# Kernel tuning notes

Hardware: AMD Instinct MI355X
Metric: run time of the kernel (lower is better)

## Reference

```python
import jax, jax.numpy as jnp
import numpy as np

B, S, D = 4, 4096, 1024
E, C, F = 8, 1024, 2048


def setup_inputs() -> dict:
    key = jax.random.key(0)
    ks = jax.random.split(key, 6)
    # weight init per module: uniform(-bound, bound), bound = sqrt(3)*sqrt(1/3)/sqrt(fan_in) = 1/sqrt(fan_in)
    b_d = 1.0 / np.sqrt(D)
    b_f = 1.0 / np.sqrt(F)
    return {
        "x": jax.random.normal(ks[0], (B, S, D), dtype=jnp.float32),
        "expert_weights": jax.random.uniform(ks[1], (B, E, C), dtype=jnp.float32),
        "token_indices": jax.random.randint(ks[2], (B, E, C), 0, S, dtype=jnp.int64),
        "w1": jax.random.uniform(ks[3], (E, D, F), dtype=jnp.float32, minval=-b_d, maxval=b_d),
        "w2": jax.random.uniform(ks[4], (E, D, F), dtype=jnp.float32, minval=-b_d, maxval=b_d),
        "w3": jax.random.uniform(ks[5], (E, F, D), dtype=jnp.float32, minval=-b_f, maxval=b_f),
    }


def reference(x, expert_weights, token_indices, w1, w2, w3):
    # gather: each expert picks `capacity` tokens from its batch row
    b_idx = jnp.arange(B)[:, None, None]                      # (B,1,1)
    expert_inputs = x[b_idx, token_indices]                   # (B,E,C,D)
    # grouped swiglu FFN per expert (no weight repeat needed: einsum batches over E)
    gate = jax.nn.silu(jnp.einsum('becd,edf->becf', expert_inputs, w1))
    value = jnp.einsum('becd,edf->becf', expert_inputs, w2)
    expert_outputs = jnp.einsum('becf,efd->becd', gate * value, w3)  # (B,E,C,D)
    weighted = expert_outputs * expert_weights[..., None]     # (B,E,C,D)
    # weighted scatter-add combine back to (B,S,D)
    out = jnp.zeros((B, S, D), dtype=x.dtype)
    out = out.at[b_idx, token_indices].add(weighted)
    return out
```

## Files before the change

### kernel.cpp

```cpp
#include <hip/hip_runtime.h>

#define Bn 4
#define Sn 4096
#define Dn 1024
#define En 8
#define Cn 1024
#define Fn 2048
#define Mn (Bn * Cn)

typedef __bf16 bf16x4 __attribute__((ext_vector_type(4)));
typedef __bf16 bf16x8 __attribute__((ext_vector_type(8)));
typedef float f32x4 __attribute__((ext_vector_type(4)));

#define GLOAD16(gsrc, ldst)                                                    \
  __builtin_amdgcn_global_load_lds(                                            \
      (const __attribute__((address_space(1))) void*)(gsrc),                   \
      (__attribute__((address_space(3))) void*)(ldst), 16, 0, 0)

#define VMCNT(n) asm volatile("s_waitcnt vmcnt(" #n ")" ::: "memory")
#define SCHEDB() __builtin_amdgcn_sched_barrier(0)

__global__ __launch_bounds__(256) void tcast_kernel(
    const float* __restrict__ in, __bf16* __restrict__ out, int K, int N) {
  __shared__ float t[32][33];
  const int e = blockIdx.z;
  const float* src = in + (size_t)e * K * N;
  __bf16* dst = out + (size_t)e * K * N;
  const int n0 = blockIdx.x << 5, k0 = blockIdx.y << 5;
  const int tx = threadIdx.x & 31, ty = threadIdx.x >> 5;
#pragma unroll
  for (int i = 0; i < 4; ++i)
    t[ty + i * 8][tx] = src[(size_t)(k0 + ty + i * 8) * N + (n0 + tx)];
  __syncthreads();
#pragma unroll
  for (int i = 0; i < 4; ++i)
    dst[(size_t)(n0 + ty + i * 8) * K + (k0 + tx)] = (__bf16)t[tx][ty + i * 8];
}

__global__ __launch_bounds__(256) void gather_cast_kernel(
    const float* __restrict__ x, const int* __restrict__ tok,
    __bf16* __restrict__ Xg) {
  const int gid = blockIdx.x * 4 + (threadIdx.x >> 6);
  const int lane = threadIdx.x & 63;
  const int e = gid >> 12, m = gid & 4095, b = m >> 10, c = m & 1023;
  const int t = tok[((size_t)b * En + e) * Cn + c];
  const float* src = x + ((size_t)b * Sn + t) * Dn;
  __bf16* dst = Xg + (size_t)gid * Dn;
#pragma unroll
  for (int i = 0; i < 4; ++i) {
    f32x4 v = *(const f32x4*)(src + i * 256 + lane * 4);
    bf16x4 o;
    o[0] = (__bf16)v[0];
    o[1] = (__bf16)v[1];
    o[2] = (__bf16)v[2];
    o[3] = (__bf16)v[3];
    *(bf16x4*)(dst + i * 256 + lane * 4) = o;
  }
}

__global__ __launch_bounds__(512, 2) void gemm12_kernel(
    const __bf16* __restrict__ Xg, const float* __restrict__ ew,
    const __bf16* __restrict__ w1T, const __bf16* __restrict__ w2T,
    __bf16* __restrict__ Hbh, int e0) {
  __shared__ __align__(16) char lds[131072];
  __bf16* As = (__bf16*)lds;
  __bf16* Bs = (__bf16*)(lds + 65536);
  float* xch = (float*)lds;

  const int tid = threadIdx.x;
  const int lane = tid & 63, wid = tid >> 6;
  const int wr = wid >> 2, wc = wid & 3;
  const int mt = blockIdx.x, ft = blockIdx.y, eLoc = blockIdx.z;
  const int e = e0 + eLoc;

  const int srow = tid >> 2;
  const int sof = ((tid & 3) ^ ((tid >> 3) & 3)) << 3;

  const __bf16* pA0 = Xg + ((size_t)e * Mn + mt * 256 + srow) * Dn + sof;
  const __bf16* pA1 = pA0 + (size_t)128 * Dn;
  const __bf16* pB0 = w1T + ((size_t)e * Fn + ft * 128 + srow) * Dn + sof;
  const __bf16* pB1 = w2T + ((size_t)e * Fn + ft * 128 + srow) * Dn + sof;

  f32x4 acc[8][4];
  const f32x4 z4 = {0.f, 0.f, 0.f, 0.f};
#pragma unroll
  for (int i = 0; i < 8; ++i)
#pragma unroll
    for (int j = 0; j < 4; ++j) acc[i][j] = z4;

  auto stage = [&](int kt) {
    const int buf = kt & 3;
    const int ko = kt << 5;
    GLOAD16(pA0 + ko, As + buf * 8192 + wid * 512);
    GLOAD16(pA1 + ko, As + buf * 8192 + 4096 + wid * 512);
    GLOAD16(pB0 + ko, Bs + buf * 8192 + wid * 512);
    GLOAD16(pB1 + ko, Bs + buf * 8192 + 4096 + wid * 512);
  };

  const int kb = lane >> 4, rl = lane & 15;
  auto compute = [&](int buf) {
    const __bf16* Ab = As + buf * 8192;
    const __bf16* Bb = Bs + buf * 8192;
    bf16x8 a8[8], b8[4];
#pragma unroll
    for (int fm = 0; fm < 8; ++fm) {
      const int r = wr * 128 + fm * 16 + rl;
      a8[fm] = *(const bf16x8*)(Ab + r * 32 + ((kb ^ ((r >> 1) & 3)) << 3));
    }
#pragma unroll
    for (int fn = 0; fn < 4; ++fn) {
      const int r = wc * 64 + fn * 16 + rl;
      b8[fn] = *(const bf16x8*)(Bb + r * 32 + ((kb ^ ((r >> 1) & 3)) << 3));
    }
    __builtin_amdgcn_s_setprio(1);
#pragma unroll
    for (int fm = 0; fm < 8; ++fm)
#pragma unroll
      for (int fn = 0; fn < 4; ++fn)
        acc[fm][fn] = __builtin_amdgcn_mfma_f32_16x16x32_bf16(
            a8[fm], b8[fn], acc[fm][fn], 0, 0, 0);
    __builtin_amdgcn_s_setprio(0);
  };

  const int KT = Dn / 32;
  stage(0);
  stage(1);
  stage(2);
#pragma unroll 1
  for (int kt = 0; kt < KT; ++kt) {
    SCHEDB();
    if (kt < KT - 2)
      VMCNT(8);
    else if (kt == KT - 2)
      VMCNT(4);
    else
      VMCNT(0);
    __builtin_amdgcn_s_barrier();
    SCHEDB();
    if (kt + 3 < KT) stage(kt + 3);
    compute(kt & 3);
  }

  __syncthreads();
  const int rl0 = (lane >> 4) << 2, cl = lane & 15;
  if (wc >= 2) {
    float* reg = xch + (wr * 2 + (wc - 2)) * 8192;
#pragma unroll
    for (int fm = 0; fm < 8; ++fm)
#pragma unroll
      for (int fn = 0; fn < 4; ++fn)
#pragma unroll
        for (int j = 0; j < 4; ++j) {
          const int row = fm * 16 + rl0 + j;
          reg[row * 64 + ((fn ^ ((row >> 2) & 3)) << 4) + cl] = acc[fm][fn][j];
        }
  }
  __syncthreads();
  if (wc < 2) {
    const float* reg = xch + (wr * 2 + wc) * 8192;
    const int m0 = mt * 256 + wr * 128;
    const int b = m0 >> 10;
    const size_t ewBase = ((size_t)b * En + e) * Cn;
    __bf16* hOut =
        Hbh + ((size_t)eLoc * Mn + m0) * Fn + ft * 128 + wc * 64;
#pragma unroll
    for (int fm = 0; fm < 8; ++fm)
#pragma unroll
      for (int j = 0; j < 4; ++j) {
        const int rloc = fm * 16 + rl0 + j;
        const float wgt = ew[ewBase + ((m0 + rloc) & (Cn - 1))];
#pragma unroll
        for (int fn = 0; fn < 4; ++fn) {
          const float g = acc[fm][fn][j];
          const float v = reg[rloc * 64 + ((fn ^ ((rloc >> 2) & 3)) << 4) + cl];
          const float h = (g / (1.f + __expf(-g))) * v * wgt;
          hOut[(size_t)rloc * Fn + fn * 16 + cl] = (__bf16)h;
        }
      }
  }
}

__global__ __launch_bounds__(512, 2) void gemm3_kernel(
    const __bf16* __restrict__ Hbh, const __bf16* __restrict__ w3T,
    const int* __restrict__ tok, float* __restrict__ out, int e0) {
  __shared__ __align__(16) char lds[131072];
  __bf16* As = (__bf16*)lds;
  __bf16* Bs = (__bf16*)(lds + 65536);

  const int tid = threadIdx.x;
  const int lane = tid & 63, wid = tid >> 6;
  const int wr = wid >> 2, wc = wid & 3;
  const int mt = blockIdx.x, nt = blockIdx.y, eLoc = blockIdx.z;
  const int e = e0 + eLoc;

  const int srow = tid >> 2;
  const int sof = ((tid & 3) ^ ((tid >> 3) & 3)) << 3;

  const __bf16* pA0 = Hbh + ((size_t)eLoc * Mn + mt * 256 + srow) * Fn + sof;
  const __bf16* pA1 = pA0 + (size_t)128 * Fn;
  const __bf16* pB0 = w3T + ((size_t)e * Dn + nt * 256 + srow) * Fn + sof;
  const __bf16* pB1 = pB0 + (size_t)128 * Fn;

  f32x4 acc[8][4];
  const f32x4 z4 = {0.f, 0.f, 0.f, 0.f};
#pragma unroll
  for (int i = 0; i < 8; ++i)
#pragma unroll
    for (int j = 0; j < 4; ++j) acc[i][j] = z4;

  auto stage = [&](int kt) {
    const int buf = kt & 3;
    const int ko = kt << 5;
    GLOAD16(pA0 + ko, As + buf * 8192 + wid * 512);
    GLOAD16(pA1 + ko, As + buf * 8192 + 4096 + wid * 512);
    GLOAD16(pB0 + ko, Bs + buf * 8192 + wid * 512);
    GLOAD16(pB1 + ko, Bs + buf * 8192 + 4096 + wid * 512);
  };

  const int kb = lane >> 4, rl = lane & 15;
  auto compute = [&](int buf) {
    const __bf16* Ab = As + buf * 8192;
    const __bf16* Bb = Bs + buf * 8192;
    bf16x8 a8[8], b8[4];
#pragma unroll
    for (int fm = 0; fm < 8; ++fm) {
      const int r = wr * 128 + fm * 16 + rl;
      a8[fm] = *(const bf16x8*)(Ab + r * 32 + ((kb ^ ((r >> 1) & 3)) << 3));
    }
#pragma unroll
    for (int fn = 0; fn < 4; ++fn) {
      const int r = wc * 64 + fn * 16 + rl;
      b8[fn] = *(const bf16x8*)(Bb + r * 32 + ((kb ^ ((r >> 1) & 3)) << 3));
    }
    __builtin_amdgcn_s_setprio(1);
#pragma unroll
    for (int fm = 0; fm < 8; ++fm)
#pragma unroll
      for (int fn = 0; fn < 4; ++fn)
        acc[fm][fn] = __builtin_amdgcn_mfma_f32_16x16x32_bf16(
            a8[fm], b8[fn], acc[fm][fn], 0, 0, 0);
    __builtin_amdgcn_s_setprio(0);
  };

  const int KT = Fn / 32;
  stage(0);
  stage(1);
  stage(2);
#pragma unroll 1
  for (int kt = 0; kt < KT; ++kt) {
    SCHEDB();
    if (kt < KT - 2)
      VMCNT(8);
    else if (kt == KT - 2)
      VMCNT(4);
    else
      VMCNT(0);
    __builtin_amdgcn_s_barrier();
    SCHEDB();
    if (kt + 3 < KT) stage(kt + 3);
    compute(kt & 3);
  }

  const int m0 = mt * 256 + wr * 128;
  const int b = m0 >> 10;
  const int rl0 = (lane >> 4) << 2, cl = lane & 15;
  const int colBase = nt * 256 + wc * 64 + cl;
#pragma unroll
  for (int fm = 0; fm < 8; ++fm) {
#pragma unroll
    for (int j = 0; j < 4; ++j) {
      const int m = m0 + fm * 16 + rl0 + j;
      const int c = m & (Cn - 1);
      const int t = tok[((size_t)b * En + e) * Cn + c];
      float* orow = out + ((size_t)b * Sn + t) * Dn + colBase;
#pragma unroll
      for (int fn = 0; fn < 4; ++fn)
        atomicAdd(orow + fn * 16, acc[fm][fn][j]);
    }
  }
}

extern "C" void kernel_launch(void* const* d_in, const int* in_sizes, int n_in,
                              void* d_out, int out_size, void* d_ws,
                              size_t ws_size, hipStream_t stream) {
  const float* x = (const float*)d_in[0];
  const float* ew = (const float*)d_in[1];
  const int* tok = (const int*)d_in[2];
  const float* w1 = (const float*)d_in[3];
  const float* w2 = (const float*)d_in[4];
  const float* w3 = (const float*)d_in[5];
  float* out = (float*)d_out;

  const size_t wE = (size_t)En * Dn * Fn;
  const size_t xgE = (size_t)En * Mn * Dn;
  const size_t hbE = (size_t)(En / 2) * Mn * Fn;
  __bf16* w1T = (__bf16*)d_ws;
  __bf16* w2T = w1T + wE;
  __bf16* w3T = w2T + wE;
  __bf16* Xg = w3T + wE;
  __bf16* Hbh = Xg + xgE;
  const size_t need = (3 * wE + xgE + hbE) * sizeof(__bf16);
  if (ws_size < need) return;

  (void)hipMemsetAsync(d_out, 0, (size_t)Bn * Sn * Dn * sizeof(float), stream);

  tcast_kernel<<<dim3(Fn / 32, Dn / 32, En), 256, 0, stream>>>(w1, w1T, Dn, Fn);
  tcast_kernel<<<dim3(Fn / 32, Dn / 32, En), 256, 0, stream>>>(w2, w2T, Dn, Fn);
  tcast_kernel<<<dim3(Dn / 32, Fn / 32, En), 256, 0, stream>>>(w3, w3T, Fn, Dn);
  gather_cast_kernel<<<dim3(En * Mn / 4), 256, 0, stream>>>(x, tok, Xg);
  for (int h = 0; h < 2; ++h) {
    gemm12_kernel<<<dim3(16, 16, En / 2), 512, 0, stream>>>(Xg, ew, w1T, w2T,
                                                            Hbh, h * (En / 2));
    gemm3_kernel<<<dim3(16, 4, En / 2), 512, 0, stream>>>(Hbh, w3T, tok, out,
                                                          h * (En / 2));
  }
}
```

Baseline: 662.9 us.

## Restructure GEMM main loops into 8-wave ping-pong schedule with split LDS reads

```diff
diff --git a/kernel.cpp b/kernel.cpp
--- a/kernel.cpp
+++ b/kernel.cpp
@@ -18,7 +18,10 @@
       (__attribute__((address_space(3))) void*)(ldst), 16, 0, 0)
 
 #define VMCNT(n) asm volatile("s_waitcnt vmcnt(" #n ")" ::: "memory")
+#define LGKM0() asm volatile("s_waitcnt lgkmcnt(0)" ::: "memory")
 #define SCHEDB() __builtin_amdgcn_sched_barrier(0)
+#define SBAR() __builtin_amdgcn_s_barrier()
+#define PRIO(p) __builtin_amdgcn_s_setprio(p)
 
 __global__ __launch_bounds__(256) void tcast_kernel(
     const float* __restrict__ in, __bf16* __restrict__ out, int K, int N) {
@@ -58,13 +61,12 @@
   }
 }
 
+
 __global__ __launch_bounds__(512, 2) void gemm12_kernel(
     const __bf16* __restrict__ Xg, const float* __restrict__ ew,
     const __bf16* __restrict__ w1T, const __bf16* __restrict__ w2T,
     __bf16* __restrict__ Hbh, int e0) {
   __shared__ __align__(16) char lds[131072];
-  __bf16* As = (__bf16*)lds;
-  __bf16* Bs = (__bf16*)(lds + 65536);
   float* xch = (float*)lds;
 
   const int tid = threadIdx.x;
@@ -75,12 +77,32 @@
 
   const int srow = tid >> 2;
   const int sof = ((tid & 3) ^ ((tid >> 3) & 3)) << 3;
-
   const __bf16* pA0 = Xg + ((size_t)e * Mn + mt * 256 + srow) * Dn + sof;
   const __bf16* pA1 = pA0 + (size_t)128 * Dn;
   const __bf16* pB0 = w1T + ((size_t)e * Fn + ft * 128 + srow) * Dn + sof;
   const __bf16* pB1 = w2T + ((size_t)e * Fn + ft * 128 + srow) * Dn + sof;
 
+  char* sA = lds + tid * 16;
+  char* sB = lds + 65536 + tid * 16;
+
+  auto stageA = [&](int src, int par, int kh) {
+    const int ko = (src << 6) + (kh << 5);
+    char* d = sA + ((par * 2 + kh) << 14);
+    GLOAD16(pA0 + ko, d);
+    GLOAD16(pA1 + ko, d + 8192);
+  };
+  auto stageB = [&](int src, int par, int kh) {
+    const int ko = (src << 6) + (kh << 5);
+    char* d = sB + ((par * 2 + kh) << 14);
+    GLOAD16(pB0 + ko, d);
+    GLOAD16(pB1 + ko, d + 8192);
+  };
+
+  const int rl = lane & 15, kb = lane >> 4;
+  const int swz = (kb ^ ((rl >> 1) & 3)) << 4;
+  const char* aLane = lds + (wr * 128 + rl) * 64 + swz;
+  const char* bLane = lds + 65536 + (wc * 64 + rl) * 64 + swz;
+
   f32x4 acc[8][4];
   const f32x4 z4 = {0.f, 0.f, 0.f, 0.f};
 #pragma unroll
@@ -88,60 +110,67 @@
 #pragma unroll
     for (int j = 0; j < 4; ++j) acc[i][j] = z4;
 
-  auto stage = [&](int kt) {
-    const int buf = kt & 3;
-    const int ko = kt << 5;
-    GLOAD16(pA0 + ko, As + buf * 8192 + wid * 512);
-    GLOAD16(pA1 + ko, As + buf * 8192 + 4096 + wid * 512);
-    GLOAD16(pB0 + ko, Bs + buf * 8192 + wid * 512);
-    GLOAD16(pB1 + ko, Bs + buf * 8192 + 4096 + wid * 512);
-  };
-
-  const int kb = lane >> 4, rl = lane & 15;
-  auto compute = [&](int buf) {
-    const __bf16* Ab = As + buf * 8192;
-    const __bf16* Bb = Bs + buf * 8192;
-    bf16x8 a8[8], b8[4];
-#pragma unroll
-    for (int fm = 0; fm < 8; ++fm) {
-      const int r = wr * 128 + fm * 16 + rl;
-      a8[fm] = *(const bf16x8*)(Ab + r * 32 + ((kb ^ ((r >> 1) & 3)) << 3));
-    }
-#pragma unroll
-    for (int fn = 0; fn < 4; ++fn) {
-      const int r = wc * 64 + fn * 16 + rl;
-      b8[fn] = *(const bf16x8*)(Bb + r * 32 + ((kb ^ ((r >> 1) & 3)) << 3));
-    }
-    __builtin_amdgcn_s_setprio(1);
-#pragma unroll
-    for (int fm = 0; fm < 8; ++fm)
-#pragma unroll
-      for (int fn = 0; fn < 4; ++fn)
-        acc[fm][fn] = __builtin_amdgcn_mfma_f32_16x16x32_bf16(
-            a8[fm], b8[fn], acc[fm][fn], 0, 0, 0);
-    __builtin_amdgcn_s_setprio(0);
-  };
-
-  const int KT = Dn / 32;
-  stage(0);
-  stage(1);
-  stage(2);
+  bf16x8 a4[4], b4[4];
+  auto readA = [&](int par, int ks, int fh) {
+    const char* p = aLane + ((par * 2 + ks) << 14) + (fh << 12);
+#pragma unroll
+    for (int i = 0; i < 4; ++i) a4[i] = *(const bf16x8*)(p + (i << 10));
+  };
+  auto readB = [&](int par, int ks) {
+    const char* p = bLane + ((par * 2 + ks) << 14);
+#pragma unroll
+    for (int i = 0; i < 4; ++i) b4[i] = *(const bf16x8*)(p + (i << 10));
+  };
+  auto mfma16 = [&](int fh) {
+    PRIO(1);
+#pragma unroll
+    for (int i = 0; i < 4; ++i)
+#pragma unroll
+      for (int j = 0; j < 4; ++j)
+        acc[fh * 4 + i][j] = __builtin_amdgcn_mfma_f32_16x16x32_bf16(
+            a4[i], b4[j], acc[fh * 4 + i][j], 0, 0, 0);
+    PRIO(0);
+  };
+
+  stageB(0, 0, 0); stageA(0, 0, 0); stageB(0, 0, 1); stageA(0, 0, 1);
+  stageB(1, 1, 0); stageA(1, 1, 0); stageB(1, 1, 1);
+  VMCNT(6);
+  SBAR();
+  SCHEDB();
+
+  const int KT = Dn >> 6;
 #pragma unroll 1
-  for (int kt = 0; kt < KT; ++kt) {
-    SCHEDB();
-    if (kt < KT - 2)
-      VMCNT(8);
-    else if (kt == KT - 2)
-      VMCNT(4);
-    else
-      VMCNT(0);
-    __builtin_amdgcn_s_barrier();
-    SCHEDB();
-    if (kt + 3 < KT) stage(kt + 3);
-    compute(kt & 3);
-  }
-
+  for (int c = 0; c < KT; ++c) {
+    const int par = c & 1;
+    const int n1 = (c + 1 < KT) ? c + 1 : KT - 1;
+    const int n2 = (c + 2 < KT) ? c + 2 : KT - 1;
+    readA(par, 0, 0);
+    readB(par, 0);
+    stageA(n1, par ^ 1, 1);
+    SBAR(); LGKM0(); SCHEDB();
+    mfma16(0);
+    SBAR(); SCHEDB();
+    readA(par, 0, 1);
+    stageB(n2, par, 0);
+    SBAR(); LGKM0(); SCHEDB();
+    mfma16(1);
+    SBAR(); SCHEDB();
+    readA(par, 1, 0);
+    readB(par, 1);
+    stageA(n2, par, 0);
+    SBAR(); LGKM0(); SCHEDB();
+    mfma16(0);
+    SBAR(); SCHEDB();
+    readA(par, 1, 1);
+    stageB(n2, par, 1);
+    SBAR(); LGKM0(); SCHEDB();
+    mfma16(1);
+    VMCNT(6);
+    SBAR(); SCHEDB();
+  }
+  VMCNT(0);
   __syncthreads();
+
   const int rl0 = (lane >> 4) << 2, cl = lane & 15;
   if (wc >= 2) {
     float* reg = xch + (wr * 2 + (wc - 2)) * 8192;
@@ -161,8 +190,7 @@
     const int m0 = mt * 256 + wr * 128;
     const int b = m0 >> 10;
     const size_t ewBase = ((size_t)b * En + e) * Cn;
-    __bf16* hOut =
-        Hbh + ((size_t)eLoc * Mn + m0) * Fn + ft * 128 + wc * 64;
+    __bf16* hOut = Hbh + ((size_t)eLoc * Mn + m0) * Fn + ft * 128 + wc * 64;
 #pragma unroll
     for (int fm = 0; fm < 8; ++fm)
 #pragma unroll
@@ -184,8 +212,6 @@
     const __bf16* __restrict__ Hbh, const __bf16* __restrict__ w3T,
     const int* __restrict__ tok, float* __restrict__ out, int e0) {
   __shared__ __align__(16) char lds[131072];
-  __bf16* As = (__bf16*)lds;
-  __bf16* Bs = (__bf16*)(lds + 65536);
 
   const int tid = threadIdx.x;
   const int lane = tid & 63, wid = tid >> 6;
@@ -195,12 +221,32 @@
 
   const int srow = tid >> 2;
   const int sof = ((tid & 3) ^ ((tid >> 3) & 3)) << 3;
-
   const __bf16* pA0 = Hbh + ((size_t)eLoc * Mn + mt * 256 + srow) * Fn + sof;
   const __bf16* pA1 = pA0 + (size_t)128 * Fn;
   const __bf16* pB0 = w3T + ((size_t)e * Dn + nt * 256 + srow) * Fn + sof;
   const __bf16* pB1 = pB0 + (size_t)128 * Fn;
 
+  char* sA = lds + tid * 16;
+  char* sB = lds + 65536 + tid * 16;
+
+  auto stageA = [&](int src, int par, int kh) {
+    const int ko = (src << 6) + (kh << 5);
+    char* d = sA + ((par * 2 + kh) << 14);
+    GLOAD16(pA0 + ko, d);
+    GLOAD16(pA1 + ko, d + 8192);
+  };
+  auto stageB = [&](int src, int par, int kh) {
+    const int ko = (src << 6) + (kh << 5);
+    char* d = sB + ((par * 2 + kh) << 14);
+    GLOAD16(pB0 + ko, d);
+    GLOAD16(pB1 + ko, d + 8192);
+  };
+
+  const int rl = lane & 15, kb = lane >> 4;
+  const int swz = (kb ^ ((rl >> 1) & 3)) << 4;
+  const char* aLane = lds + (wr * 128 + rl) * 64 + swz;
+  const char* bLane = lds + 65536 + (wc * 64 + rl) * 64 + swz;
+
   f32x4 acc[8][4];
   const f32x4 z4 = {0.f, 0.f, 0.f, 0.f};
 #pragma unroll
@@ -208,58 +254,65 @@
 #pragma unroll
     for (int j = 0; j < 4; ++j) acc[i][j] = z4;
 
-  auto stage = [&](int kt) {
-    const int buf = kt & 3;
-    const int ko = kt << 5;
-    GLOAD16(pA0 + ko, As + buf * 8192 + wid * 512);
-    GLOAD16(pA1 + ko, As + buf * 8192 + 4096 + wid * 512);
-    GLOAD16(pB0 + ko, Bs + buf * 8192 + wid * 512);
-    GLOAD16(pB1 + ko, Bs + buf * 8192 + 4096 + wid * 512);
-  };
-
-  const int kb = lane >> 4, rl = lane & 15;
-  auto compute = [&](int buf) {
-    const __bf16* Ab = As + buf * 8192;
-    const __bf16* Bb = Bs + buf * 8192;
-    bf16x8 a8[8], b8[4];
-#pragma unroll
-    for (int fm = 0; fm < 8; ++fm) {
-      const int r = wr * 128 + fm * 16 + rl;
-      a8[fm] = *(const bf16x8*)(Ab + r * 32 + ((kb ^ ((r >> 1) & 3)) << 3));
-    }
-#pragma unroll
-    for (int fn = 0; fn < 4; ++fn) {
-      const int r = wc * 64 + fn * 16 + rl;
-      b8[fn] = *(const bf16x8*)(Bb + r * 32 + ((kb ^ ((r >> 1) & 3)) << 3));
-    }
-    __builtin_amdgcn_s_setprio(1);
-#pragma unroll
-    for (int fm = 0; fm < 8; ++fm)
-#pragma unroll
-      for (int fn = 0; fn < 4; ++fn)
-        acc[fm][fn] = __builtin_amdgcn_mfma_f32_16x16x32_bf16(
-            a8[fm], b8[fn], acc[fm][fn], 0, 0, 0);
-    __builtin_amdgcn_s_setprio(0);
-  };
-
-  const int KT = Fn / 32;
-  stage(0);
-  stage(1);
-  stage(2);
+  bf16x8 a4[4], b4[4];
+  auto readA = [&](int par, int ks, int fh) {
+    const char* p = aLane + ((par * 2 + ks) << 14) + (fh << 12);
+#pragma unroll
+    for (int i = 0; i < 4; ++i) a4[i] = *(const bf16x8*)(p + (i << 10));
+  };
+  auto readB = [&](int par, int ks) {
+    const char* p = bLane + ((par * 2 + ks) << 14);
+#pragma unroll
+    for (int i = 0; i < 4; ++i) b4[i] = *(const bf16x8*)(p + (i << 10));
+  };
+  auto mfma16 = [&](int fh) {
+    PRIO(1);
+#pragma unroll
+    for (int i = 0; i < 4; ++i)
+#pragma unroll
+      for (int j = 0; j < 4; ++j)
+        acc[fh * 4 + i][j] = __builtin_amdgcn_mfma_f32_16x16x32_bf16(
+            a4[i], b4[j], acc[fh * 4 + i][j], 0, 0, 0);
+    PRIO(0);
+  };
+
+  stageB(0, 0, 0); stageA(0, 0, 0); stageB(0, 0, 1); stageA(0, 0, 1);
+  stageB(1, 1, 0); stageA(1, 1, 0); stageB(1, 1, 1);
+  VMCNT(6);
+  SBAR();
+  SCHEDB();
+
+  const int KT = Fn >> 6;
 #pragma unroll 1
-  for (int kt = 0; kt < KT; ++kt) {
-    SCHEDB();
-    if (kt < KT - 2)
-      VMCNT(8);
-    else if (kt == KT - 2)
-      VMCNT(4);
-    else
-      VMCNT(0);
-    __builtin_amdgcn_s_barrier();
-    SCHEDB();
-    if (kt + 3 < KT) stage(kt + 3);
-    compute(kt & 3);
-  }
+  for (int c = 0; c < KT; ++c) {
+    const int par = c & 1;
+    const int n1 = (c + 1 < KT) ? c + 1 : KT - 1;
+    const int n2 = (c + 2 < KT) ? c + 2 : KT - 1;
+    readA(par, 0, 0);
+    readB(par, 0);
+    stageA(n1, par ^ 1, 1);
+    SBAR(); LGKM0(); SCHEDB();
+    mfma16(0);
+    SBAR(); SCHEDB();
+    readA(par, 0, 1);
+    stageB(n2, par, 0);
+    SBAR(); LGKM0(); SCHEDB();
+    mfma16(1);
+    SBAR(); SCHEDB();
+    readA(par, 1, 0);
+    readB(par, 1);
+    stageA(n2, par, 0);
+    SBAR(); LGKM0(); SCHEDB();
+    mfma16(0);
+    SBAR(); SCHEDB();
+    readA(par, 1, 1);
+    stageB(n2, par, 1);
+    SBAR(); LGKM0(); SCHEDB();
+    mfma16(1);
+    VMCNT(6);
+    SBAR(); SCHEDB();
+  }
+  VMCNT(0);
 
   const int m0 = mt * 256 + wr * 128;
   const int b = m0 >> 10;
@@ -270,8 +323,8 @@
 #pragma unroll
     for (int j = 0; j < 4; ++j) {
       const int m = m0 + fm * 16 + rl0 + j;
-      const int c = m & (Cn - 1);
-      const int t = tok[((size_t)b * En + e) * Cn + c];
+      const int c2 = m & (Cn - 1);
+      const int t = tok[((size_t)b * En + e) * Cn + c2];
       float* orow = out + ((size_t)b * Sn + t) * Dn + colBase;
 #pragma unroll
       for (int fn = 0; fn < 4; ++fn)
```

New measurement: 660.7 us. No clear change (-0.3%).

## Shrink GEMM tiles to 128 rows with double-buffered LDS for higher occupancy

Applied to the files above, without the earlier changes.

```diff
diff --git a/kernel.cpp b/kernel.cpp
--- a/kernel.cpp
+++ b/kernel.cpp
@@ -17,8 +17,7 @@
       (const __attribute__((address_space(1))) void*)(gsrc),                   \
       (__attribute__((address_space(3))) void*)(ldst), 16, 0, 0)
 
-#define VMCNT(n) asm volatile("s_waitcnt vmcnt(" #n ")" ::: "memory")
-#define SCHEDB() __builtin_amdgcn_sched_barrier(0)
+#define VMCNT0() asm volatile("s_waitcnt vmcnt(0)" ::: "memory")
 
 __global__ __launch_bounds__(256) void tcast_kernel(
     const float* __restrict__ in, __bf16* __restrict__ out, int K, int N) {
@@ -58,14 +57,12 @@
   }
 }
 
-__global__ __launch_bounds__(512, 2) void gemm12_kernel(
+
+__global__ __launch_bounds__(512, 4) void gemm12_kernel(
     const __bf16* __restrict__ Xg, const float* __restrict__ ew,
     const __bf16* __restrict__ w1T, const __bf16* __restrict__ w2T,
     __bf16* __restrict__ Hbh, int e0) {
-  __shared__ __align__(16) char lds[131072];
-  __bf16* As = (__bf16*)lds;
-  __bf16* Bs = (__bf16*)(lds + 65536);
-  float* xch = (float*)lds;
+  __shared__ __align__(16) char lds[49152];
 
   const int tid = threadIdx.x;
   const int lane = tid & 63, wid = tid >> 6;
@@ -75,117 +72,112 @@
 
   const int srow = tid >> 2;
   const int sof = ((tid & 3) ^ ((tid >> 3) & 3)) << 3;
-
-  const __bf16* pA0 = Xg + ((size_t)e * Mn + mt * 256 + srow) * Dn + sof;
-  const __bf16* pA1 = pA0 + (size_t)128 * Dn;
-  const __bf16* pB0 = w1T + ((size_t)e * Fn + ft * 128 + srow) * Dn + sof;
-  const __bf16* pB1 = w2T + ((size_t)e * Fn + ft * 128 + srow) * Dn + sof;
-
-  f32x4 acc[8][4];
+  const __bf16* pA = Xg + ((size_t)e * Mn + mt * 128 + srow) * Dn + sof;
+  const __bf16* pB1 = w1T + ((size_t)e * Fn + ft * 128 + srow) * Dn + sof;
+  const __bf16* pB2 = w2T + ((size_t)e * Fn + ft * 128 + srow) * Dn + sof;
+
+  auto stage = [&](int slot) {
+    char* d = lds + slot * 24576 + tid * 16;
+    GLOAD16(pA, d);
+    GLOAD16(pB1, d + 8192);
+    GLOAD16(pB2, d + 16384);
+    pA += 32;
+    pB1 += 32;
+    pB2 += 32;
+  };
+
+  const int rl = lane & 15, kb = lane >> 4;
+  const int swz = (kb ^ ((rl >> 1) & 3)) << 4;
+
+  f32x4 acc[4][4];
   const f32x4 z4 = {0.f, 0.f, 0.f, 0.f};
 #pragma unroll
-  for (int i = 0; i < 8; ++i)
+  for (int i = 0; i < 4; ++i)
 #pragma unroll
     for (int j = 0; j < 4; ++j) acc[i][j] = z4;
 
-  auto stage = [&](int kt) {
-    const int buf = kt & 3;
-    const int ko = kt << 5;
-    GLOAD16(pA0 + ko, As + buf * 8192 + wid * 512);
-    GLOAD16(pA1 + ko, As + buf * 8192 + 4096 + wid * 512);
-    GLOAD16(pB0 + ko, Bs + buf * 8192 + wid * 512);
-    GLOAD16(pB1 + ko, Bs + buf * 8192 + 4096 + wid * 512);
-  };
-
-  const int kb = lane >> 4, rl = lane & 15;
-  auto compute = [&](int buf) {
-    const __bf16* Ab = As + buf * 8192;
-    const __bf16* Bb = Bs + buf * 8192;
-    bf16x8 a8[8], b8[4];
-#pragma unroll
-    for (int fm = 0; fm < 8; ++fm) {
-      const int r = wr * 128 + fm * 16 + rl;
-      a8[fm] = *(const bf16x8*)(Ab + r * 32 + ((kb ^ ((r >> 1) & 3)) << 3));
+  stage(0);
+  VMCNT0();
+  __syncthreads();
+
+  const int KT = Dn / 32;
+#pragma unroll 1
+  for (int c = 0; c < KT; ++c) {
+    if (c + 1 < KT) stage((c + 1) & 1);
+    const char* Ab = lds + (c & 1) * 24576;
+    const char* Bb = Ab + 8192;
+    bf16x8 a4[4], b4[4];
+#pragma unroll
+    for (int f = 0; f < 4; ++f) {
+      const int ra = wr * 64 + f * 16 + rl;
+      a4[f] = *(const bf16x8*)(Ab + ra * 64 + swz);
+      const int rb = wc * 64 + f * 16 + rl;
+      b4[f] = *(const bf16x8*)(Bb + rb * 64 + swz);
     }
 #pragma unroll
-    for (int fn = 0; fn < 4; ++fn) {
-      const int r = wc * 64 + fn * 16 + rl;
-      b8[fn] = *(const bf16x8*)(Bb + r * 32 + ((kb ^ ((r >> 1) & 3)) << 3));
-    }
-    __builtin_amdgcn_s_setprio(1);
-#pragma unroll
-    for (int fm = 0; fm < 8; ++fm)
+    for (int fm = 0; fm < 4; ++fm)
 #pragma unroll
       for (int fn = 0; fn < 4; ++fn)
         acc[fm][fn] = __builtin_amdgcn_mfma_f32_16x16x32_bf16(
-            a8[fm], b8[fn], acc[fm][fn], 0, 0, 0);
-    __builtin_amdgcn_s_setprio(0);
-  };
-
-  const int KT = Dn / 32;
-  stage(0);
-  stage(1);
-  stage(2);
-#pragma unroll 1
-  for (int kt = 0; kt < KT; ++kt) {
-    SCHEDB();
-    if (kt < KT - 2)
-      VMCNT(8);
-    else if (kt == KT - 2)
-      VMCNT(4);
-    else
-      VMCNT(0);
-    __builtin_amdgcn_s_barrier();
-    SCHEDB();
-    if (kt + 3 < KT) stage(kt + 3);
-    compute(kt & 3);
-  }
-
-  __syncthreads();
+            a4[fm], b4[fn], acc[fm][fn], 0, 0, 0);
+    __syncthreads();
+  }
+
   const int rl0 = (lane >> 4) << 2, cl = lane & 15;
   if (wc >= 2) {
-    float* reg = xch + (wr * 2 + (wc - 2)) * 8192;
-#pragma unroll
-    for (int fm = 0; fm < 8; ++fm)
+    char* reg = lds + (wr * 2 + (wc - 2)) * 8192;
+#pragma unroll
+    for (int fm = 0; fm < 4; ++fm)
 #pragma unroll
       for (int fn = 0; fn < 4; ++fn)
 #pragma unroll
         for (int j = 0; j < 4; ++j) {
           const int row = fm * 16 + rl0 + j;
-          reg[row * 64 + ((fn ^ ((row >> 2) & 3)) << 4) + cl] = acc[fm][fn][j];
+          *(__bf16*)(reg + row * 128 + ((fn ^ ((row >> 2) & 3)) << 5) +
+                     cl * 2) = (__bf16)acc[fm][fn][j];
         }
   }
   __syncthreads();
   if (wc < 2) {
-    const float* reg = xch + (wr * 2 + wc) * 8192;
-    const int m0 = mt * 256 + wr * 128;
+    char* reg = lds + (wr * 2 + wc) * 8192;
+    const int m0 = mt * 128 + wr * 64;
     const int b = m0 >> 10;
     const size_t ewBase = ((size_t)b * En + e) * Cn;
-    __bf16* hOut =
-        Hbh + ((size_t)eLoc * Mn + m0) * Fn + ft * 128 + wc * 64;
-#pragma unroll
-    for (int fm = 0; fm < 8; ++fm)
+#pragma unroll
+    for (int fm = 0; fm < 4; ++fm)
 #pragma unroll
       for (int j = 0; j < 4; ++j) {
-        const int rloc = fm * 16 + rl0 + j;
-        const float wgt = ew[ewBase + ((m0 + rloc) & (Cn - 1))];
+        const int row = fm * 16 + rl0 + j;
+        const float wgt = ew[ewBase + ((m0 + row) & (Cn - 1))];
 #pragma unroll
         for (int fn = 0; fn < 4; ++fn) {
+          __bf16* p = (__bf16*)(reg + row * 128 +
+                                ((fn ^ ((row >> 2) & 3)) << 5) + cl * 2);
+          const float v = (float)*p;
           const float g = acc[fm][fn][j];
-          const float v = reg[rloc * 64 + ((fn ^ ((rloc >> 2) & 3)) << 4) + cl];
-          const float h = (g / (1.f + __expf(-g))) * v * wgt;
-          hOut[(size_t)rloc * Fn + fn * 16 + cl] = (__bf16)h;
+          *p = (__bf16)((g / (1.f + __expf(-g))) * v * wgt);
         }
       }
   }
-}
-
-__global__ __launch_bounds__(512, 2) void gemm3_kernel(
+  __syncthreads();
+  __bf16* hBase = Hbh + ((size_t)eLoc * Mn + mt * 128) * Fn + ft * 128;
+#pragma unroll
+  for (int p = 0; p < 4; ++p) {
+    const int row = p * 32 + (tid >> 4);
+    const int c8 = (tid & 15) * 8;
+    const int reg = (row >> 6) * 2 + (c8 >> 6);
+    const int rr = row & 63, cc = c8 & 63;
+    bf16x8 v = *(const bf16x8*)(lds + reg * 8192 + rr * 128 +
+                                (((cc >> 4) ^ ((rr >> 2) & 3)) << 5) +
+                                (cc & 15) * 2);
+    *(bf16x8*)(hBase + (size_t)row * Fn + c8) = v;
+  }
+}
+
+__global__ __launch_bounds__(512, 4) void gemm3_kernel(
     const __bf16* __restrict__ Hbh, const __bf16* __restrict__ w3T,
     const int* __restrict__ tok, float* __restrict__ out, int e0) {
-  __shared__ __align__(16) char lds[131072];
-  __bf16* As = (__bf16*)lds;
-  __bf16* Bs = (__bf16*)(lds + 65536);
+  __shared__ __align__(16) char lds[49152];
 
   const int tid = threadIdx.x;
   const int lane = tid & 63, wid = tid >> 6;
@@ -195,83 +187,68 @@
 
   const int srow = tid >> 2;
   const int sof = ((tid & 3) ^ ((tid >> 3) & 3)) << 3;
-
-  const __bf16* pA0 = Hbh + ((size_t)eLoc * Mn + mt * 256 + srow) * Fn + sof;
-  const __bf16* pA1 = pA0 + (size_t)128 * Fn;
+  const __bf16* pA = Hbh + ((size_t)eLoc * Mn + mt * 128 + srow) * Fn + sof;
   const __bf16* pB0 = w3T + ((size_t)e * Dn + nt * 256 + srow) * Fn + sof;
   const __bf16* pB1 = pB0 + (size_t)128 * Fn;
 
-  f32x4 acc[8][4];
+  auto stage = [&](int slot) {
+    char* d = lds + slot * 24576 + tid * 16;
+    GLOAD16(pA, d);
+    GLOAD16(pB0, d + 8192);
+    GLOAD16(pB1, d + 16384);
+    pA += 32;
+    pB0 += 32;
+    pB1 += 32;
+  };
+
+  const int rl = lane & 15, kb = lane >> 4;
+  const int swz = (kb ^ ((rl >> 1) & 3)) << 4;
+
+  f32x4 acc[4][4];
   const f32x4 z4 = {0.f, 0.f, 0.f, 0.f};
 #pragma unroll
-  for (int i = 0; i < 8; ++i)
+  for (int i = 0; i < 4; ++i)
 #pragma unroll
     for (int j = 0; j < 4; ++j) acc[i][j] = z4;
 
-  auto stage = [&](int kt) {
-    const int buf = kt & 3;
-    const int ko = kt << 5;
-    GLOAD16(pA0 + ko, As + buf * 8192 + wid * 512);
-    GLOAD16(pA1 + ko, As + buf * 8192 + 4096 + wid * 512);
-    GLOAD16(pB0 + ko, Bs + buf * 8192 + wid * 512);
-    GLOAD16(pB1 + ko, Bs + buf * 8192 + 4096 + wid * 512);
-  };
-
-  const int kb = lane >> 4, rl = lane & 15;
-  auto compute = [&](int buf) {
-    const __bf16* Ab = As + buf * 8192;
-    const __bf16* Bb = Bs + buf * 8192;
-    bf16x8 a8[8], b8[4];
-#pragma unroll
-    for (int fm = 0; fm < 8; ++fm) {
-      const int r = wr * 128 + fm * 16 + rl;
-      a8[fm] = *(const bf16x8*)(Ab + r * 32 + ((kb ^ ((r >> 1) & 3)) << 3));
+  stage(0);
+  VMCNT0();
+  __syncthreads();
+
+  const int KT = Fn / 32;
+#pragma unroll 1
+  for (int c = 0; c < KT; ++c) {
+    if (c + 1 < KT) stage((c + 1) & 1);
+    const char* Ab = lds + (c & 1) * 24576;
+    const char* Bb = Ab + 8192;
+    bf16x8 a4[4], b4[4];
+#pragma unroll
+    for (int f = 0; f < 4; ++f) {
+      const int ra = wr * 64 + f * 16 + rl;
+      a4[f] = *(const bf16x8*)(Ab + ra * 64 + swz);
+      const int rb = wc * 64 + f * 16 + rl;
+      b4[f] = *(const bf16x8*)(Bb + rb * 64 + swz);
     }
 #pragma unroll
-    for (int fn = 0; fn < 4; ++fn) {
-      const int r = wc * 64 + fn * 16 + rl;
-      b8[fn] = *(const bf16x8*)(Bb + r * 32 + ((kb ^ ((r >> 1) & 3)) << 3));
-    }
-    __builtin_amdgcn_s_setprio(1);
-#pragma unroll
-    for (int fm = 0; fm < 8; ++fm)
+    for (int fm = 0; fm < 4; ++fm)
 #pragma unroll
       for (int fn = 0; fn < 4; ++fn)
         acc[fm][fn] = __builtin_amdgcn_mfma_f32_16x16x32_bf16(
-            a8[fm], b8[fn], acc[fm][fn], 0, 0, 0);
-    __builtin_amdgcn_s_setprio(0);
-  };
-
-  const int KT = Fn / 32;
-  stage(0);
-  stage(1);
-  stage(2);
-#pragma unroll 1
-  for (int kt = 0; kt < KT; ++kt) {
-    SCHEDB();
-    if (kt < KT - 2)
-      VMCNT(8);
-    else if (kt == KT - 2)
-      VMCNT(4);
-    else
-      VMCNT(0);
-    __builtin_amdgcn_s_barrier();
-    SCHEDB();
-    if (kt + 3 < KT) stage(kt + 3);
-    compute(kt & 3);
-  }
-
-  const int m0 = mt * 256 + wr * 128;
+            a4[fm], b4[fn], acc[fm][fn], 0, 0, 0);
+    __syncthreads();
+  }
+
+  const int m0 = mt * 128 + wr * 64;
   const int b = m0 >> 10;
   const int rl0 = (lane >> 4) << 2, cl = lane & 15;
   const int colBase = nt * 256 + wc * 64 + cl;
 #pragma unroll
-  for (int fm = 0; fm < 8; ++fm) {
+  for (int fm = 0; fm < 4; ++fm) {
 #pragma unroll
     for (int j = 0; j < 4; ++j) {
       const int m = m0 + fm * 16 + rl0 + j;
-      const int c = m & (Cn - 1);
-      const int t = tok[((size_t)b * En + e) * Cn + c];
+      const int c2 = m & (Cn - 1);
+      const int t = tok[((size_t)b * En + e) * Cn + c2];
       float* orow = out + ((size_t)b * Sn + t) * Dn + colBase;
 #pragma unroll
       for (int fn = 0; fn < 4; ++fn)
@@ -309,9 +286,9 @@
   tcast_kernel<<<dim3(Dn / 32, Fn / 32, En), 256, 0, stream>>>(w3, w3T, Fn, Dn);
   gather_cast_kernel<<<dim3(En * Mn / 4), 256, 0, stream>>>(x, tok, Xg);
   for (int h = 0; h < 2; ++h) {
-    gemm12_kernel<<<dim3(16, 16, En / 2), 512, 0, stream>>>(Xg, ew, w1T, w2T,
+    gemm12_kernel<<<dim3(32, 16, En / 2), 512, 0, stream>>>(Xg, ew, w1T, w2T,
                                                             Hbh, h * (En / 2));
-    gemm3_kernel<<<dim3(16, 4, En / 2), 512, 0, stream>>>(Hbh, w3T, tok, out,
+    gemm3_kernel<<<dim3(32, 4, En / 2), 512, 0, stream>>>(Hbh, w3T, tok, out,
                                                           h * (En / 2));
   }
 }
```

After: 678.0 us. 1.02x slower.
